# Kernel tuning notes

Measured on AMD Instinct MI355X. Metric: run time of the kernel, lower is better.

Reference implementation:

```python
import jax, jax.numpy as jnp
import numpy as np

BETA_VQ = 0.25
NUM_CODES = 1024
CODE_DIM = 256

def setup_inputs() -> dict:
    key = jax.random.key(0)
    k1, k2 = jax.random.split(key)
    z_e = jax.random.normal(k1, (64, 32, 32, CODE_DIM), dtype=jnp.float32)
    codebook = jax.random.uniform(k2, (NUM_CODES, CODE_DIM), dtype=jnp.float32,
                                  minval=-1.0 / NUM_CODES, maxval=1.0 / NUM_CODES)
    return {"z_e": z_e, "codebook": codebook}


def reference(z_e, codebook):
    B, H, W, D = z_e.shape
    z_flat = z_e.reshape(-1, D)  # [N, D], N = B*H*W
    # squared-euclidean distances via expansion: ||z||^2 + ||c||^2 - 2 z.c
    dist = (jnp.sum(z_flat ** 2, axis=1, keepdims=True)
            + jnp.sum(codebook ** 2, axis=1)
            - 2.0 * z_flat @ codebook.T)  # [N, num_codes]
    indices = jnp.argmin(dist, axis=1)  # [N]
    z_q = codebook[indices].reshape(z_e.shape)  # [B,H,W,D]
    codebook_loss = jnp.mean((jax.lax.stop_gradient(z_e) - z_q) ** 2)
    commit_loss = BETA_VQ * jnp.mean((z_e - jax.lax.stop_gradient(z_q)) ** 2)
    vq_loss = codebook_loss + commit_loss
    z_q_st = z_e + jax.lax.stop_gradient(z_q - z_e)  # straight-through
    indices = indices.reshape(B, H, W)
    return (z_q_st, vq_loss, indices)
```

## Files before the change

### kernel.cpp

```cpp
#include <hip/hip_runtime.h>
#include <hip/hip_bf16.h>


constexpr int D     = 256;
constexpr int NC    = 1024;
constexpr int NROWS = 65536;
constexpr int RPB   = 32;
constexpr int NBLK  = NROWS / RPB;
constexpr int ZS    = 264;
constexpr int QCAP  = 512;
#define MARGIN 3e-3f

typedef float accv4  __attribute__((ext_vector_type(4)));
typedef short short8 __attribute__((ext_vector_type(8)));

__device__ __forceinline__ short f2bf(float x) {
    __hip_bfloat16 h = __float2bfloat16(x);
    return *reinterpret_cast<short*>(&h);
}
__device__ __forceinline__ unsigned packtrunc(float x, float y) {
    return (__float_as_uint(x) >> 16) | (__float_as_uint(y) & 0xffff0000u);
}

__device__ __forceinline__ float np_pairwise_sq128(const float* __restrict__ x) {
    float r[8];
    #pragma unroll
    for (int j = 0; j < 8; ++j) r[j] = __fmul_rn(x[j], x[j]);
    #pragma unroll
    for (int i = 8; i < 128; i += 8)
        #pragma unroll
        for (int j = 0; j < 8; ++j)
            r[j] = __fadd_rn(r[j], __fmul_rn(x[i + j], x[i + j]));
    float s01 = __fadd_rn(r[0], r[1]);
    float s23 = __fadd_rn(r[2], r[3]);
    float s45 = __fadd_rn(r[4], r[5]);
    float s67 = __fadd_rn(r[6], r[7]);
    return __fadd_rn(__fadd_rn(s01, s23), __fadd_rn(s45, s67));
}

__global__ void c2_kernel(const float* __restrict__ cb, float* __restrict__ c2) {
    int t = blockIdx.x * blockDim.x + threadIdx.x;
    if (t < NC) {
        const float* x = cb + (size_t)t * D;
        c2[t] = __fadd_rn(np_pairwise_sq128(x), np_pairwise_sq128(x + 128));
    }
}

__global__ void swz_kernel(const float* __restrict__ cb, short* __restrict__ swz) {
    int t = blockIdx.x * blockDim.x + threadIdx.x;
    int lane = t & 63, ts = t >> 6;
    int ks = ts & 7, tile = ts >> 3;
    int code = tile * 16 + (lane & 15);
    int kb   = ks * 32 + (lane >> 4) * 8;
    const float* src = cb + (size_t)code * D + kb;
    union { short s[8]; short8 v; } u;
    #pragma unroll
    for (int j = 0; j < 8; ++j) u.s[j] = f2bf(src[j]);
    *((short8*)swz + t) = u.v;
}

__global__ __launch_bounds__(256, 2) void vq_kernel(
    const float* __restrict__ z,
    const float* __restrict__ cb,
    const short* __restrict__ cb_swz,
    const float* __restrict__ c2g,
    float*       __restrict__ out_zq,
    float*       __restrict__ out_idx,
    double*      __restrict__ partials)
{
    __shared__ __align__(16) float z_lds[RPB][ZS];
    __shared__ float a_row[RPB];
    __shared__ __align__(16) float scratchA[RPB][4];
    __shared__ float c2_lds[NC];
    __shared__ int   rm_shared[RPB];
    __shared__ __align__(16) int queue[QCAP];
    __shared__ int   qn;

    const int tid     = threadIdx.x;
    const int lane    = tid & 63;
    const int w       = tid >> 6;
    const int rowBase = blockIdx.x * RPB;

    #pragma unroll
    for (int j = 0; j < 8; ++j) {
        int l = tid + 256 * j;
        int row = l >> 6, q = l & 63;
        float4 v = *(const float4*)(z + (size_t)(rowBase + row) * D + q * 4);
        *(float4*)&z_lds[row][q * 4] = v;
    }
    #pragma unroll
    for (int j = 0; j < 4; ++j) c2_lds[tid + 256 * j] = c2g[tid + 256 * j];
    if (tid < RPB) rm_shared[tid] = 0x7f800000;
    if (tid == 0)  qn = 0;
    __syncthreads();

    if (tid < RPB * 4) {
        int row = tid >> 2, q = tid & 3;
        int h = (q >> 1) * 128, p = (q & 1) * 4;
        const float* x = &z_lds[row][0];
        float r0 = __fmul_rn(x[h+p+0], x[h+p+0]);
        float r1 = __fmul_rn(x[h+p+1], x[h+p+1]);
        float r2 = __fmul_rn(x[h+p+2], x[h+p+2]);
        float r3 = __fmul_rn(x[h+p+3], x[h+p+3]);
        #pragma unroll
        for (int i = 8; i < 128; i += 8) {
            r0 = __fadd_rn(r0, __fmul_rn(x[h+i+p+0], x[h+i+p+0]));
            r1 = __fadd_rn(r1, __fmul_rn(x[h+i+p+1], x[h+i+p+1]));
            r2 = __fadd_rn(r2, __fmul_rn(x[h+i+p+2], x[h+i+p+2]));
            r3 = __fadd_rn(r3, __fmul_rn(x[h+i+p+3], x[h+i+p+3]));
        }
        scratchA[row][q] = __fadd_rn(__fadd_rn(r0, r1), __fadd_rn(r2, r3));
    }
    __syncthreads();
    if (tid < RPB) {
        float half0 = __fadd_rn(scratchA[tid][0], scratchA[tid][1]);
        float half1 = __fadd_rn(scratchA[tid][2], scratchA[tid][3]);
        a_row[tid]  = __fadd_rn(half0, half1);
    }
    __syncthreads();

    short8 afrag[2][8];
    #pragma unroll
    for (int rt = 0; rt < 2; ++rt)
        #pragma unroll
        for (int ks = 0; ks < 8; ++ks) {
            const float* src = z + (size_t)(rowBase + rt * 16 + (lane & 15)) * D
                                 + ks * 32 + (lane >> 4) * 8;
            float4 v0 = *(const float4*)(src);
            float4 v1 = *(const float4*)(src + 4);
            union { unsigned u[4]; short8 v; } pk;
            pk.u[0] = packtrunc(v0.x, v0.y);
            pk.u[1] = packtrunc(v0.z, v0.w);
            pk.u[2] = packtrunc(v1.x, v1.y);
            pk.u[3] = packtrunc(v1.z, v1.w);
            afrag[rt][ks] = pk.v;
        }
    float a_reg[2][4];
    #pragma unroll
    for (int rt = 0; rt < 2; ++rt)
        #pragma unroll
        for (int i = 0; i < 4; ++i)
            a_reg[rt][i] = a_row[rt * 16 + (lane >> 4) * 4 + i];

    float runmin[2][4], thr[2][4];
    #pragma unroll
    for (int rt = 0; rt < 2; ++rt)
        #pragma unroll
        for (int i = 0; i < 4; ++i) runmin[rt][i] = 3.4e38f;

    const short8* bbase = (const short8*)cb_swz + lane;
    for (int pass = 0; pass < 2; ++pass) {
        short8 bcur[8];
        #pragma unroll
        for (int ks = 0; ks < 8; ++ks) bcur[ks] = bbase[(size_t)w * 512 + ks * 64];
        for (int t = 0; t < 16; ++t) {
            int tile = w + 4 * t;
            short8 bnxt[8];
            if (t < 15) {
                int ntile = tile + 4;
                #pragma unroll
                for (int ks = 0; ks < 8; ++ks)
                    bnxt[ks] = bbase[(size_t)ntile * 512 + ks * 64];
            }
            accv4 acc[2];
            #pragma unroll
            for (int rt = 0; rt < 2; ++rt) acc[rt] = (accv4){0.f, 0.f, 0.f, 0.f};
            #pragma unroll
            for (int ks = 0; ks < 8; ++ks) {
                #pragma unroll
                for (int rt = 0; rt < 2; ++rt)
                    acc[rt] = __builtin_amdgcn_mfma_f32_16x16x32_bf16(
                        afrag[rt][ks], bcur[ks], acc[rt], 0, 0, 0);
            }
            int   col  = lane & 15;
            int   code = tile * 16 + col;
            float c2v  = c2_lds[code];
            #pragma unroll
            for (int rt = 0; rt < 2; ++rt)
                #pragma unroll
                for (int i = 0; i < 4; ++i) {
                    float key = (a_reg[rt][i] + c2v) - 2.0f * acc[rt][i];
                    if (pass == 0) {
                        runmin[rt][i] = fminf(runmin[rt][i], key);
                    } else if (key <= thr[rt][i]) {
                        int row  = rt * 16 + (lane >> 4) * 4 + i;
                        int slot = atomicAdd(&qn, 1);
                        if (slot < QCAP) queue[slot] = (row << 10) | code;
                    }
                }
            #pragma unroll
            for (int ks = 0; ks < 8; ++ks) bcur[ks] = bnxt[ks];
        }
        if (pass == 0) {
            #pragma unroll
            for (int rt = 0; rt < 2; ++rt)
                #pragma unroll
                for (int i = 0; i < 4; ++i) {
                    float m = runmin[rt][i];
                    m = fminf(m, __shfl_xor(m, 1));
                    m = fminf(m, __shfl_xor(m, 2));
                    m = fminf(m, __shfl_xor(m, 4));
                    m = fminf(m, __shfl_xor(m, 8));
                    if ((lane & 15) == 0) {
                        int row = rt * 16 + (lane >> 4) * 4 + i;
                        atomicMin(&rm_shared[row], __float_as_int(m));
                    }
                }
            __syncthreads();
            #pragma unroll
            for (int rt = 0; rt < 2; ++rt)
                #pragma unroll
                for (int i = 0; i < 4; ++i) {
                    int row = rt * 16 + (lane >> 4) * 4 + i;
                    thr[rt][i] = __int_as_float(rm_shared[row]) + MARGIN;
                }
        }
    }

    unsigned long long* best64 = (unsigned long long*)&scratchA[0][0];
    if (tid < RPB) best64[tid] = ~0ull;
    __syncthreads();
    int total = qn;
    if (total <= QCAP) {
        for (int t = tid; t < total; t += 256) {
            int e = queue[t];
            int row = e >> 10, code = e & 1023;
            const float4* cp = (const float4*)(cb + (size_t)code * D);
            const float*  zr = &z_lds[row][0];
            float acc = 0.0f;
            #pragma unroll 8
            for (int d4 = 0; d4 < 64; ++d4) {
                float4 cv = cp[d4];
                acc = fmaf(zr[d4 * 4 + 0], cv.x, acc);
                acc = fmaf(zr[d4 * 4 + 1], cv.y, acc);
                acc = fmaf(zr[d4 * 4 + 2], cv.z, acc);
                acc = fmaf(zr[d4 * 4 + 3], cv.w, acc);
            }
            float key = __fsub_rn(__fadd_rn(a_row[row], c2_lds[code]), 2.0f * acc);
            unsigned long long pk =
                ((unsigned long long)__float_as_uint(key) << 32) | (unsigned)code;
            atomicMin(&best64[row], pk);
        }
    } else {
        for (int r = 0; r < RPB; ++r) {
            for (int c = tid; c < NC; c += 256) {
                const float4* cp = (const float4*)(cb + (size_t)c * D);
                const float*  zr = &z_lds[r][0];
                float acc = 0.0f;
                #pragma unroll 8
                for (int d4 = 0; d4 < 64; ++d4) {
                    float4 cv = cp[d4];
                    acc = fmaf(zr[d4 * 4 + 0], cv.x, acc);
                    acc = fmaf(zr[d4 * 4 + 1], cv.y, acc);
                    acc = fmaf(zr[d4 * 4 + 2], cv.z, acc);
                    acc = fmaf(zr[d4 * 4 + 3], cv.w, acc);
                }
                float key = __fsub_rn(__fadd_rn(a_row[r], c2_lds[c]), 2.0f * acc);
                unsigned long long pk =
                    ((unsigned long long)__float_as_uint(key) << 32) | (unsigned)c;
                atomicMin(&best64[r], pk);
            }
        }
    }
    __syncthreads();

    int* winner = rm_shared;
    if (tid < RPB) {
        unsigned long long b = best64[tid];
        int wdx = (b == ~0ull) ? 0 : (int)(b & 0xffffffffu);
        winner[tid] = wdx;
        out_idx[rowBase + tid] = (float)wdx;
    }
    __syncthreads();

    double lacc = 0.0;
    #pragma unroll
    for (int j = 0; j < 8; ++j) {
        int idx = tid + 256 * j;
        int row = idx >> 6;
        int q4  = idx & 63;
        int wd  = winner[row];
        float4 cv = *(const float4*)(cb + (size_t)wd * D + q4 * 4);
        float4 zv = *(const float4*)&z_lds[row][q4 * 4];
        float4 o;
        o.x = __fadd_rn(zv.x, __fsub_rn(cv.x, zv.x));
        o.y = __fadd_rn(zv.y, __fsub_rn(cv.y, zv.y));
        o.z = __fadd_rn(zv.z, __fsub_rn(cv.z, zv.z));
        o.w = __fadd_rn(zv.w, __fsub_rn(cv.w, zv.w));
        *(float4*)(out_zq + (size_t)(rowBase + row) * D + q4 * 4) = o;
        double d0 = (double)zv.x - (double)cv.x;
        double d1 = (double)zv.y - (double)cv.y;
        double d2 = (double)zv.z - (double)cv.z;
        double d3 = (double)zv.w - (double)cv.w;
        lacc += d0 * d0 + d1 * d1 + d2 * d2 + d3 * d3;
    }
    __syncthreads();
    double* dred = (double*)&queue[0];
    dred[tid] = lacc;
    __syncthreads();
    for (int s = 128; s > 0; s >>= 1) {
        if (tid < s) dred[tid] += dred[tid + s];
        __syncthreads();
    }
    if (tid == 0) partials[blockIdx.x] = dred[0];
}

__global__ void loss_kernel(const double* __restrict__ partials,
                            float* __restrict__ out_loss)
{
    __shared__ double sm[256];
    int tid = threadIdx.x;
    double s = 0.0;
    for (int i = tid; i < NBLK; i += 256) s += partials[i];
    sm[tid] = s;
    __syncthreads();
    for (int k = 128; k > 0; k >>= 1) {
        if (tid < k) sm[tid] += sm[tid + k];
        __syncthreads();
    }
    if (tid == 0)
        out_loss[0] = (float)(1.25 * sm[0] / (double)((size_t)NROWS * D));
}

extern "C" void kernel_launch(void* const* d_in, const int* in_sizes, int n_in,
                              void* d_out, int out_size, void* d_ws, size_t ws_size,
                              hipStream_t stream)
{
    const float* z  = (const float*)d_in[0];
    const float* cb = (const float*)d_in[1];

    float* out      = (float*)d_out;
    float* out_zq   = out;
    float* out_loss = out + (size_t)NROWS * D;
    float* out_idx  = out_loss + 1;

    char*   ws       = (char*)d_ws;
    short*  cb_swz   = (short*)ws;
    float*  c2       = (float*)(ws + 524288);
    double* partials = (double*)(ws + 528384);

    swz_kernel<<<128, 256, 0, stream>>>(cb, cb_swz);
    c2_kernel<<<4, 256, 0, stream>>>(cb, c2);
    vq_kernel<<<NBLK, 256, 0, stream>>>(z, cb, cb_swz, c2,
                                        out_zq, out_idx, partials);
    loss_kernel<<<1, 256, 0, stream>>>(partials, out_loss);
}
```

Measured before the change: 254.8 us.

## Replace two-pass distance GEMM with single pass caching bf16-packed keys in registers

The codebook scan previously ran the MFMA distance computation twice, once to find each row's minimum and again to queue candidates within a margin. The new code runs it once, stores the per-tile partial keys (2*z·c - ||c||²) truncated to bf16 and packed two per register, then does candidate selection from those registers after the row-minimum reduction. The truncation loses precision, so the margin is widened to compensate. This halves the MFMA work and codebook streaming, but costs many extra VGPRs (64 packed words), which may reduce occupancy or cause spills. A wider margin can also mean more queued candidates for exact rescoring.

```diff
diff --git a/kernel.cpp b/kernel.cpp
--- a/kernel.cpp
+++ b/kernel.cpp
@@ -9,7 +9,7 @@
 constexpr int NBLK  = NROWS / RPB;
 constexpr int ZS    = 264;
 constexpr int QCAP  = 512;
-#define MARGIN 3e-3f
+#define MARGIN_Q 3.8e-3f
 
 typedef float accv4  __attribute__((ext_vector_type(4)));
 typedef short short8 __attribute__((ext_vector_type(8)));
@@ -142,79 +142,103 @@
         for (int i = 0; i < 4; ++i)
             a_reg[rt][i] = a_row[rt * 16 + (lane >> 4) * 4 + i];
 
-    float runmin[2][4], thr[2][4];
+    float runmin[2][4];
     #pragma unroll
     for (int rt = 0; rt < 2; ++rt)
         #pragma unroll
         for (int i = 0; i < 4; ++i) runmin[rt][i] = 3.4e38f;
 
+    unsigned kpk[16][2][2];
     const short8* bbase = (const short8*)cb_swz + lane;
-    for (int pass = 0; pass < 2; ++pass) {
-        short8 bcur[8];
-        #pragma unroll
-        for (int ks = 0; ks < 8; ++ks) bcur[ks] = bbase[(size_t)w * 512 + ks * 64];
-        for (int t = 0; t < 16; ++t) {
-            int tile = w + 4 * t;
-            short8 bnxt[8];
-            if (t < 15) {
-                int ntile = tile + 4;
-                #pragma unroll
-                for (int ks = 0; ks < 8; ++ks)
-                    bnxt[ks] = bbase[(size_t)ntile * 512 + ks * 64];
-            }
-            accv4 acc[2];
+    short8 bcur[8];
+    #pragma unroll
+    for (int ks = 0; ks < 8; ++ks) bcur[ks] = bbase[(size_t)w * 512 + ks * 64];
+
+    #pragma unroll
+    for (int t = 0; t < 16; ++t) {
+        const int tile = w + 4 * t;
+        short8 bnxt[8];
+        if (t < 15) {
             #pragma unroll
-            for (int rt = 0; rt < 2; ++rt) acc[rt] = (accv4){0.f, 0.f, 0.f, 0.f};
-            #pragma unroll
-            for (int ks = 0; ks < 8; ++ks) {
-                #pragma unroll
-                for (int rt = 0; rt < 2; ++rt)
-                    acc[rt] = __builtin_amdgcn_mfma_f32_16x16x32_bf16(
-                        afrag[rt][ks], bcur[ks], acc[rt], 0, 0, 0);
-            }
-            int   col  = lane & 15;
-            int   code = tile * 16 + col;
-            float c2v  = c2_lds[code];
+            for (int ks = 0; ks < 8; ++ks)
+                bnxt[ks] = bbase[(size_t)(tile + 4) * 512 + ks * 64];
+        }
+        accv4 acc[2];
+        #pragma unroll
+        for (int rt = 0; rt < 2; ++rt) acc[rt] = (accv4){0.f, 0.f, 0.f, 0.f};
+        #pragma unroll
+        for (int ks = 0; ks < 8; ++ks) {
             #pragma unroll
             for (int rt = 0; rt < 2; ++rt)
-                #pragma unroll
-                for (int i = 0; i < 4; ++i) {
-                    float key = (a_reg[rt][i] + c2v) - 2.0f * acc[rt][i];
-                    if (pass == 0) {
-                        runmin[rt][i] = fminf(runmin[rt][i], key);
-                    } else if (key <= thr[rt][i]) {
-                        int row  = rt * 16 + (lane >> 4) * 4 + i;
-                        int slot = atomicAdd(&qn, 1);
-                        if (slot < QCAP) queue[slot] = (row << 10) | code;
-                    }
-                }
+                acc[rt] = __builtin_amdgcn_mfma_f32_16x16x32_bf16(
+                    afrag[rt][ks], bcur[ks], acc[rt], 0, 0, 0);
+        }
+        const float c2v = c2_lds[tile * 16 + (lane & 15)];
+        #pragma unroll
+        for (int rt = 0; rt < 2; ++rt) {
+            float m0 = fmaf(2.0f, acc[rt][0], -c2v);
+            float m1 = fmaf(2.0f, acc[rt][1], -c2v);
+            float m2 = fmaf(2.0f, acc[rt][2], -c2v);
+            float m3 = fmaf(2.0f, acc[rt][3], -c2v);
+            kpk[t][rt][0] = packtrunc(m0, m1);
+            kpk[t][rt][1] = packtrunc(m2, m3);
+            runmin[rt][0] = fminf(runmin[rt][0], a_reg[rt][0] - m0);
+            runmin[rt][1] = fminf(runmin[rt][1], a_reg[rt][1] - m1);
+            runmin[rt][2] = fminf(runmin[rt][2], a_reg[rt][2] - m2);
+            runmin[rt][3] = fminf(runmin[rt][3], a_reg[rt][3] - m3);
+        }
+        if (t < 15) {
             #pragma unroll
             for (int ks = 0; ks < 8; ++ks) bcur[ks] = bnxt[ks];
         }
-        if (pass == 0) {
+    }
+
+    #pragma unroll
+    for (int rt = 0; rt < 2; ++rt)
+        #pragma unroll
+        for (int i = 0; i < 4; ++i) {
+            float m = runmin[rt][i];
+            m = fminf(m, __shfl_xor(m, 1));
+            m = fminf(m, __shfl_xor(m, 2));
+            m = fminf(m, __shfl_xor(m, 4));
+            m = fminf(m, __shfl_xor(m, 8));
+            if ((lane & 15) == 0) {
+                int row = rt * 16 + (lane >> 4) * 4 + i;
+                atomicMin(&rm_shared[row], __float_as_int(m));
+            }
+        }
+    __syncthreads();
+
+    float mthr[2][4];
+    #pragma unroll
+    for (int rt = 0; rt < 2; ++rt)
+        #pragma unroll
+        for (int i = 0; i < 4; ++i) {
+            int row = rt * 16 + (lane >> 4) * 4 + i;
+            mthr[rt][i] = a_reg[rt][i]
+                        - (__int_as_float(rm_shared[row]) + MARGIN_Q);
+        }
+    #pragma unroll
+    for (int t = 0; t < 16; ++t) {
+        const int code = (w + 4 * t) * 16 + (lane & 15);
+        #pragma unroll
+        for (int rt = 0; rt < 2; ++rt)
             #pragma unroll
-            for (int rt = 0; rt < 2; ++rt)
-                #pragma unroll
-                for (int i = 0; i < 4; ++i) {
-                    float m = runmin[rt][i];
-                    m = fminf(m, __shfl_xor(m, 1));
-                    m = fminf(m, __shfl_xor(m, 2));
-                    m = fminf(m, __shfl_xor(m, 4));
-                    m = fminf(m, __shfl_xor(m, 8));
-                    if ((lane & 15) == 0) {
-                        int row = rt * 16 + (lane >> 4) * 4 + i;
-                        atomicMin(&rm_shared[row], __float_as_int(m));
-                    }
+            for (int pr = 0; pr < 2; ++pr) {
+                unsigned pk = kpk[t][rt][pr];
+                float mlo = __uint_as_float(pk << 16);
+                float mhi = __uint_as_float(pk & 0xffff0000u);
+                if (mlo >= mthr[rt][2 * pr]) {
+                    int row  = rt * 16 + (lane >> 4) * 4 + 2 * pr;
+                    int slot = atomicAdd(&qn, 1);
+                    if (slot < QCAP) queue[slot] = (row << 10) | code;
                 }
-            __syncthreads();
-            #pragma unroll
-            for (int rt = 0; rt < 2; ++rt)
-                #pragma unroll
-                for (int i = 0; i < 4; ++i) {
-                    int row = rt * 16 + (lane >> 4) * 4 + i;
-                    thr[rt][i] = __int_as_float(rm_shared[row]) + MARGIN;
+                if (mhi >= mthr[rt][2 * pr + 1]) {
+                    int row  = rt * 16 + (lane >> 4) * 4 + 2 * pr + 1;
+                    int slot = atomicAdd(&qn, 1);
+                    if (slot < QCAP) queue[slot] = (row << 10) | code;
                 }
-        }
+            }
     }
 
     unsigned long long* best64 = (unsigned long long*)&scratchA[0][0];
```

After: 311.7 us. 1.22x slower.

## Merge prep kernels and fold loss reduction into last-block of VQ kernel

Applied to the files above, without the earlier changes.

Fuses the codebook swizzle and squared-norm kernels into one prep launch, and replaces the separate loss-reduction kernel with a last-block-done pattern using an atomic counter, reducing four launches to two. The swizzle now uses vectorized float4 loads. It also changes the z row padding stride in LDS from 264 to 260 floats, which alters the bank-conflict pattern and LDS footprint. The atomic counter adds a fence and a serial tail reduction in one block.

```diff
diff --git a/kernel.cpp b/kernel.cpp
--- a/kernel.cpp
+++ b/kernel.cpp
@@ -7,7 +7,7 @@
 constexpr int NROWS = 65536;
 constexpr int RPB   = 32;
 constexpr int NBLK  = NROWS / RPB;
-constexpr int ZS    = 264;
+constexpr int ZS    = 260;
 constexpr int QCAP  = 512;
 #define MARGIN 3e-3f
 
@@ -38,25 +38,35 @@
     return __fadd_rn(__fadd_rn(s01, s23), __fadd_rn(s45, s67));
 }
 
-__global__ void c2_kernel(const float* __restrict__ cb, float* __restrict__ c2) {
-    int t = blockIdx.x * blockDim.x + threadIdx.x;
-    if (t < NC) {
-        const float* x = cb + (size_t)t * D;
-        c2[t] = __fadd_rn(np_pairwise_sq128(x), np_pairwise_sq128(x + 128));
-    }
-}
-
-__global__ void swz_kernel(const float* __restrict__ cb, short* __restrict__ swz) {
-    int t = blockIdx.x * blockDim.x + threadIdx.x;
-    int lane = t & 63, ts = t >> 6;
-    int ks = ts & 7, tile = ts >> 3;
-    int code = tile * 16 + (lane & 15);
-    int kb   = ks * 32 + (lane >> 4) * 8;
-    const float* src = cb + (size_t)code * D + kb;
-    union { short s[8]; short8 v; } u;
-    #pragma unroll
-    for (int j = 0; j < 8; ++j) u.s[j] = f2bf(src[j]);
-    *((short8*)swz + t) = u.v;
+__global__ void prep_kernel(const float* __restrict__ cb,
+                            short* __restrict__ swz,
+                            float* __restrict__ c2,
+                            unsigned* __restrict__ ctr)
+{
+    int b = blockIdx.x;
+    if (b < 128) {
+        int t = b * 256 + threadIdx.x;
+        int lane = t & 63, ts = t >> 6;
+        int ks = ts & 7, tile = ts >> 3;
+        int code = tile * 16 + (lane & 15);
+        int kb   = ks * 32 + (lane >> 4) * 8;
+        const float* src = cb + (size_t)code * D + kb;
+        float4 v0 = *(const float4*)(src);
+        float4 v1 = *(const float4*)(src + 4);
+        union { short s[8]; short8 v; } u;
+        u.s[0] = f2bf(v0.x); u.s[1] = f2bf(v0.y);
+        u.s[2] = f2bf(v0.z); u.s[3] = f2bf(v0.w);
+        u.s[4] = f2bf(v1.x); u.s[5] = f2bf(v1.y);
+        u.s[6] = f2bf(v1.z); u.s[7] = f2bf(v1.w);
+        *((short8*)swz + t) = u.v;
+    } else {
+        if (b == 131 && threadIdx.x == 0) *ctr = 0u;
+        int t = (b - 128) * 256 + threadIdx.x;
+        if (t < NC) {
+            const float* x = cb + (size_t)t * D;
+            c2[t] = __fadd_rn(np_pairwise_sq128(x), np_pairwise_sq128(x + 128));
+        }
+    }
 }
 
 __global__ __launch_bounds__(256, 2) void vq_kernel(
@@ -66,7 +76,9 @@
     const float* __restrict__ c2g,
     float*       __restrict__ out_zq,
     float*       __restrict__ out_idx,
-    double*      __restrict__ partials)
+    double*      __restrict__ partials,
+    float*       __restrict__ out_loss,
+    unsigned*    __restrict__ ctr)
 {
     __shared__ __align__(16) float z_lds[RPB][ZS];
     __shared__ float a_row[RPB];
@@ -75,6 +87,7 @@
     __shared__ int   rm_shared[RPB];
     __shared__ __align__(16) int queue[QCAP];
     __shared__ int   qn;
+    __shared__ int   amLast;
 
     const int tid     = threadIdx.x;
     const int lane    = tid & 63;
@@ -302,24 +315,28 @@
         if (tid < s) dred[tid] += dred[tid + s];
         __syncthreads();
     }
-    if (tid == 0) partials[blockIdx.x] = dred[0];
-}
-
-__global__ void loss_kernel(const double* __restrict__ partials,
-                            float* __restrict__ out_loss)
-{
-    __shared__ double sm[256];
-    int tid = threadIdx.x;
-    double s = 0.0;
-    for (int i = tid; i < NBLK; i += 256) s += partials[i];
-    sm[tid] = s;
-    __syncthreads();
-    for (int k = 128; k > 0; k >>= 1) {
-        if (tid < k) sm[tid] += sm[tid + k];
+
+    if (tid == 0) {
+        partials[blockIdx.x] = dred[0];
+        __threadfence();
+        unsigned old = atomicAdd(ctr, 1u);
+        amLast = (old == (unsigned)(NBLK - 1)) ? 1 : 0;
+    }
+    __syncthreads();
+    if (amLast) {
+        __threadfence();
+        double s = 0.0;
+        for (int i = tid; i < NBLK; i += 256)
+            s += atomicAdd(&partials[i], 0.0);
+        dred[tid] = s;
         __syncthreads();
-    }
-    if (tid == 0)
-        out_loss[0] = (float)(1.25 * sm[0] / (double)((size_t)NROWS * D));
+        for (int k = 128; k > 0; k >>= 1) {
+            if (tid < k) dred[tid] += dred[tid + k];
+            __syncthreads();
+        }
+        if (tid == 0)
+            out_loss[0] = (float)(1.25 * dred[0] / (double)((size_t)NROWS * D));
+    }
 }
 
 extern "C" void kernel_launch(void* const* d_in, const int* in_sizes, int n_in,
@@ -334,14 +351,14 @@
     float* out_loss = out + (size_t)NROWS * D;
     float* out_idx  = out_loss + 1;
 
-    char*   ws       = (char*)d_ws;
-    short*  cb_swz   = (short*)ws;
-    float*  c2       = (float*)(ws + 524288);
-    double* partials = (double*)(ws + 528384);
-
-    swz_kernel<<<128, 256, 0, stream>>>(cb, cb_swz);
-    c2_kernel<<<4, 256, 0, stream>>>(cb, c2);
+    char*     ws       = (char*)d_ws;
+    short*    cb_swz   = (short*)ws;
+    float*    c2       = (float*)(ws + 524288);
+    double*   partials = (double*)(ws + 528384);
+    unsigned* ctr      = (unsigned*)(ws + 544768);
+
+    prep_kernel<<<132, 256, 0, stream>>>(cb, cb_swz, c2, ctr);
     vq_kernel<<<NBLK, 256, 0, stream>>>(z, cb, cb_swz, c2,
-                                        out_zq, out_idx, partials);
-    loss_kernel<<<1, 256, 0, stream>>>(partials, out_loss);
-}
+                                        out_zq, out_idx, partials,
+                                        out_loss, ctr);
+}
```

New measurement: 325.3 us. +27.7%, slower.
